# Optimization experiments

Hardware: AMD Instinct MI355X
Metric: run time of the kernel (lower is better)

## Reference

```python
import jax, jax.numpy as jnp
import numpy as np

D_MODEL = 512
NUM_HEADS = 8
BATCH = 2
SEQ = 2048


def setup_inputs() -> dict:
    key = jax.random.key(0)
    ks = jax.random.split(key, 10)
    H = D_MODEL * NUM_HEADS  # concat width = 4096
    scale_in = 1.0 / np.sqrt(D_MODEL)
    scale_h = 1.0 / np.sqrt(H)
    inp = {
        "input_data": jax.random.normal(ks[0], (BATCH, SEQ, D_MODEL), dtype=jnp.float32),
        # causal mask, broadcastable to [n, h, q, k]; masked_fill where mask == 0
        "mask": jnp.tril(jnp.ones((SEQ, SEQ), dtype=jnp.int32))[None, None, :, :],
        "Wq": jax.random.normal(ks[1], (D_MODEL, H), dtype=jnp.float32) * scale_in,
        "bq": jnp.zeros((H,), dtype=jnp.float32),
        "Wk": jax.random.normal(ks[2], (D_MODEL, H), dtype=jnp.float32) * scale_in,
        "bk": jnp.zeros((H,), dtype=jnp.float32),
        "Wv": jax.random.normal(ks[3], (D_MODEL, H), dtype=jnp.float32) * scale_in,
        "bv": jnp.zeros((H,), dtype=jnp.float32),
        "Wo": jax.random.normal(ks[4], (H, D_MODEL), dtype=jnp.float32) * scale_h,
        "bo": jnp.zeros((D_MODEL,), dtype=jnp.float32),
    }
    return inp


def reference(input_data, mask, Wq, bq, Wk, bk, Wv, bv, Wo, bo):
    n, s, d_model = input_data.shape
    H = Wq.shape[1] // d_model  # num_heads; per-head dim == d_model in this module
    q = (input_data @ Wq + bq).reshape(n, s, H, d_model)
    k = (input_data @ Wk + bk).reshape(n, s, H, d_model)
    v = (input_data @ Wv + bv).reshape(n, s, H, d_model)
    scores = jnp.einsum('nqhd,nkhd->nhqk', q, k) / jnp.sqrt(jnp.float32(d_model))
    scores = jnp.where(mask == 0, jnp.float32(-1e9), scores)
    weights = jax.nn.softmax(scores, axis=-1)
    # Faithful to source: contracts weights over BOTH k and q axes (source quirk)
    output = jnp.einsum('nhkq,nvhd->nvhd', weights, v)
    concat = output.reshape(n, s, H * d_model)
    return concat @ Wo + bo
```

## Files before the change

### kernel.cpp

```cpp
#include <hip/hip_runtime.h>


#define DM 512
#define HC 4096
#define SEQF 2048.0f
#define LDR 40

typedef short bf16x8 __attribute__((ext_vector_type(8)));
typedef float f32x4 __attribute__((ext_vector_type(4)));

__device__ __forceinline__ void split2(float x, ushort& h, ushort& l) {
    unsigned b = __float_as_uint(x);
    h = (ushort)(b >> 16);
    float hf = __uint_as_float((unsigned)h << 16);
    l = (ushort)(__float_as_uint(x - hf) >> 16);
}

__device__ __forceinline__ void stage64_f32(const float* __restrict__ src, int ld,
                                            int row0, int k0, ushort* Hh, ushort* Hl,
                                            int tid) {
    const int r = tid >> 2, co = (tid & 3) * 8;
    const float* p = src + (size_t)(row0 + r) * ld + k0 + co;
    const float4 v0 = *reinterpret_cast<const float4*>(p);
    const float4 v1 = *reinterpret_cast<const float4*>(p + 4);
    ushort4 h0, l0, h1, l1;
    split2(v0.x, h0.x, l0.x); split2(v0.y, h0.y, l0.y);
    split2(v0.z, h0.z, l0.z); split2(v0.w, h0.w, l0.w);
    split2(v1.x, h1.x, l1.x); split2(v1.y, h1.y, l1.y);
    split2(v1.z, h1.z, l1.z); split2(v1.w, h1.w, l1.w);
    *reinterpret_cast<ushort4*>(&Hh[r * LDR + co])     = h0;
    *reinterpret_cast<ushort4*>(&Hh[r * LDR + co + 4]) = h1;
    *reinterpret_cast<ushort4*>(&Hl[r * LDR + co])     = l0;
    *reinterpret_cast<ushort4*>(&Hl[r * LDR + co + 4]) = l1;
}

__device__ __forceinline__ void stage64_bf16(const ushort* __restrict__ sh,
                                             const ushort* __restrict__ sl, int ld,
                                             int row0, int k0, ushort* Hh, ushort* Hl,
                                             int tid) {
    const int r = tid >> 2, co = (tid & 3) * 8;
    const size_t off = (size_t)(row0 + r) * ld + k0 + co;
    *reinterpret_cast<int4*>(&Hh[r * LDR + co]) = *reinterpret_cast<const int4*>(&sh[off]);
    *reinterpret_cast<int4*>(&Hl[r * LDR + co]) = *reinterpret_cast<const int4*>(&sl[off]);
}

__global__ __launch_bounds__(256) void prep_wo(const float* __restrict__ Wo,
                                               const float* __restrict__ bv,
                                               ushort* __restrict__ WoTh,
                                               ushort* __restrict__ WoTl,
                                               float* __restrict__ cvec) {
    __shared__ float T[64][65];
    const int bj = blockIdx.x;
    const int bn = blockIdx.y;
    const int tid = threadIdx.x;
    {
        const int r = tid >> 2, c16 = (tid & 3) * 16;
        const float* p = Wo + (size_t)(bj * 64 + r) * DM + bn * 64 + c16;
#pragma unroll
        for (int c = 0; c < 4; ++c) {
            float4 v = *reinterpret_cast<const float4*>(p + c * 4);
            T[r][c16 + c * 4 + 0] = v.x;
            T[r][c16 + c * 4 + 1] = v.y;
            T[r][c16 + c * 4 + 2] = v.z;
            T[r][c16 + c * 4 + 3] = v.w;
        }
    }
    __syncthreads();
    {
        const int rn = tid >> 2, c16 = (tid & 3) * 16;
        const size_t off = (size_t)(bn * 64 + rn) * HC + bj * 64 + c16;
#pragma unroll
        for (int q = 0; q < 4; ++q) {
            ushort4 uh, ul;
            split2(T[c16 + q * 4 + 0][rn], uh.x, ul.x);
            split2(T[c16 + q * 4 + 1][rn], uh.y, ul.y);
            split2(T[c16 + q * 4 + 2][rn], uh.z, ul.z);
            split2(T[c16 + q * 4 + 3][rn], uh.w, ul.w);
            *reinterpret_cast<ushort4*>(&WoTh[off + q * 4]) = uh;
            *reinterpret_cast<ushort4*>(&WoTl[off + q * 4]) = ul;
        }
    }
    if (tid < 64) {
        float s = 0.f;
#pragma unroll 8
        for (int j = 0; j < 64; ++j) s = fmaf(bv[bj * 64 + j], T[j][tid], s);
        atomicAdd(&cvec[bn * 64 + tid], SEQF * s);
    }
}

__global__ __launch_bounds__(256) void gemm_wcT(const ushort* __restrict__ WoTh,
                                                const ushort* __restrict__ WoTl,
                                                const float* __restrict__ Wv,
                                                float* __restrict__ WcT) {
    __shared__ ushort Ah[64 * LDR], Al[64 * LDR], Bh[64 * LDR], Bl[64 * LDR];
    const int d = blockIdx.x;
    const int lin = (d & 7) * 64 + (d >> 3);
    const int kc = lin >> 6, tile = lin & 63;
    const int nt = tile >> 3, it = tile & 7;
    const int a0 = nt * 64, b0 = it * 64, kb = kc * 512;
    const int tid = threadIdx.x, wave = tid >> 6, lane = tid & 63;
    const int wm = wave * 16, fr = lane & 15, fs = (lane >> 4) * 8;

    f32x4 acc[4] = {};
    for (int t = 0; t < 16; ++t) {
        const int k0 = kb + t * 32;
        stage64_bf16(WoTh, WoTl, HC, a0, k0, Ah, Al, tid);
        stage64_f32(Wv, HC, b0, k0, Bh, Bl, tid);
        __syncthreads();
        const int ai = (wm + fr) * LDR + fs;
        const bf16x8 ah = *reinterpret_cast<const bf16x8*>(&Ah[ai]);
        const bf16x8 al = *reinterpret_cast<const bf16x8*>(&Al[ai]);
#pragma unroll
        for (int g = 0; g < 4; ++g) {
            const int bi = (g * 16 + fr) * LDR + fs;
            const bf16x8 bh = *reinterpret_cast<const bf16x8*>(&Bh[bi]);
            const bf16x8 bl = *reinterpret_cast<const bf16x8*>(&Bl[bi]);
            acc[g] = __builtin_amdgcn_mfma_f32_16x16x32_bf16(ah, bh, acc[g], 0, 0, 0);
            acc[g] = __builtin_amdgcn_mfma_f32_16x16x32_bf16(ah, bl, acc[g], 0, 0, 0);
            acc[g] = __builtin_amdgcn_mfma_f32_16x16x32_bf16(al, bh, acc[g], 0, 0, 0);
        }
        __syncthreads();
    }
#pragma unroll
    for (int g = 0; g < 4; ++g)
#pragma unroll
        for (int q = 0; q < 4; ++q) {
            const int row = a0 + wm + (lane >> 4) * 4 + q;
            const int col = b0 + g * 16 + (lane & 15);
            atomicAdd(&WcT[(size_t)row * DM + col], SEQF * acc[g][q]);
        }
}

__global__ __launch_bounds__(256) void gemm_out(const float* __restrict__ X,
                                                const float* __restrict__ WcT,
                                                const float* __restrict__ cvec,
                                                const float* __restrict__ bo,
                                                float* __restrict__ out) {
    __shared__ ushort Ah[64 * LDR], Al[64 * LDR], Bh[64 * LDR], Bl[64 * LDR];
    const int d = blockIdx.x;
    const int lin = (d & 7) * 64 + (d >> 3);
    const int mt = lin >> 3, nt = lin & 7;
    const int a0 = mt * 64, b0 = nt * 64;
    const int tid = threadIdx.x, wave = tid >> 6, lane = tid & 63;
    const int wm = wave * 16, fr = lane & 15, fs = (lane >> 4) * 8;

    f32x4 acc[4] = {};
    for (int t = 0; t < 16; ++t) {
        const int k0 = t * 32;
        stage64_f32(X, DM, a0, k0, Ah, Al, tid);
        stage64_f32(WcT, DM, b0, k0, Bh, Bl, tid);
        __syncthreads();
        const int ai = (wm + fr) * LDR + fs;
        const bf16x8 ah = *reinterpret_cast<const bf16x8*>(&Ah[ai]);
        const bf16x8 al = *reinterpret_cast<const bf16x8*>(&Al[ai]);
#pragma unroll
        for (int g = 0; g < 4; ++g) {
            const int bi = (g * 16 + fr) * LDR + fs;
            const bf16x8 bh = *reinterpret_cast<const bf16x8*>(&Bh[bi]);
            const bf16x8 bl = *reinterpret_cast<const bf16x8*>(&Bl[bi]);
            acc[g] = __builtin_amdgcn_mfma_f32_16x16x32_bf16(ah, bh, acc[g], 0, 0, 0);
            acc[g] = __builtin_amdgcn_mfma_f32_16x16x32_bf16(ah, bl, acc[g], 0, 0, 0);
            acc[g] = __builtin_amdgcn_mfma_f32_16x16x32_bf16(al, bh, acc[g], 0, 0, 0);
        }
        __syncthreads();
    }
#pragma unroll
    for (int g = 0; g < 4; ++g) {
        const int n = b0 + g * 16 + (lane & 15);
        const float cb = cvec[n] + bo[n];
#pragma unroll
        for (int q = 0; q < 4; ++q) {
            const int m = a0 + wm + (lane >> 4) * 4 + q;
            out[(size_t)m * DM + n] = acc[g][q] + cb;
        }
    }
}

extern "C" void kernel_launch(void* const* d_in, const int* in_sizes, int n_in,
                              void* d_out, int out_size, void* d_ws, size_t ws_size,
                              hipStream_t stream) {
    const float* input = (const float*)d_in[0];
    const float* Wv    = (const float*)d_in[6];
    const float* bv    = (const float*)d_in[7];
    const float* Wo    = (const float*)d_in[8];
    const float* bo    = (const float*)d_in[9];
    float* out = (float*)d_out;

    ushort* WoTh = (ushort*)d_ws;
    ushort* WoTl = WoTh + (size_t)DM * HC;
    float*  WcT  = (float*)(WoTl + (size_t)DM * HC);
    float*  cvec = WcT + (size_t)DM * DM;

    hipMemsetAsync(WcT, 0, (size_t)DM * DM * 4 + DM * 4, stream);

    prep_wo<<<dim3(64, 8), 256, 0, stream>>>(Wo, bv, WoTh, WoTl, cvec);
    gemm_wcT<<<512, 256, 0, stream>>>(WoTh, WoTl, Wv, WcT);
    gemm_out<<<512, 256, 0, stream>>>(input, WcT, cvec, bo, out);
}
```

Before: 154.4 us.

## Fuse memset, Wo prep and both GEMMs into one cooperative kernel with grid syncs

Replaces the memset and three separate kernel launches with a single cooperative kernel that zeroes the workspace, transposes and splits Wo, computes WcT, then computes the output, with grid-wide syncs between phases. The GEMM loops now prefetch the next K tile into registers while the current tile is computed, a register-level software pipeline. The bias-vector reduction moves into the second phase and reads the bf16 hi/lo split of Wo from global memory. This removes launch overhead and inter-kernel gaps, at the cost of grid-sync overhead and a hard requirement that all 512 blocks are co-resident.

```diff
diff --git a/kernel.cpp b/kernel.cpp
--- a/kernel.cpp
+++ b/kernel.cpp
@@ -1,4 +1,7 @@
 #include <hip/hip_runtime.h>
+#include <hip/hip_cooperative_groups.h>
+
+namespace cg = cooperative_groups;
 
 
 #define DM 512
@@ -15,163 +18,201 @@
     float hf = __uint_as_float((unsigned)h << 16);
     l = (ushort)(__float_as_uint(x - hf) >> 16);
 }
-
-__device__ __forceinline__ void stage64_f32(const float* __restrict__ src, int ld,
-                                            int row0, int k0, ushort* Hh, ushort* Hl,
-                                            int tid) {
+__device__ __forceinline__ float bf2f(ushort u) {
+    return __uint_as_float((unsigned)u << 16);
+}
+
+__global__ __launch_bounds__(256) void fused_mha(
+    const float* __restrict__ X, const float* __restrict__ Wv,
+    const float* __restrict__ bv, const float* __restrict__ Wo,
+    const float* __restrict__ bo, ushort* __restrict__ WoTh,
+    ushort* __restrict__ WoTl, float* __restrict__ WcT,
+    float* __restrict__ cvec, float* __restrict__ out) {
+    __shared__ alignas(16) unsigned char smem[20480];
+    ushort* Ah = (ushort*)smem;
+    ushort* Al = Ah + 2560;
+    ushort* Bh = Al + 2560;
+    ushort* Bl = Bh + 2560;
+
+    const int bid = blockIdx.x, tid = threadIdx.x;
+    const int lane = tid & 63, wave = tid >> 6;
+    const int wm = wave * 16, fr = lane & 15, fs = (lane >> 4) * 8;
     const int r = tid >> 2, co = (tid & 3) * 8;
-    const float* p = src + (size_t)(row0 + r) * ld + k0 + co;
-    const float4 v0 = *reinterpret_cast<const float4*>(p);
-    const float4 v1 = *reinterpret_cast<const float4*>(p + 4);
-    ushort4 h0, l0, h1, l1;
-    split2(v0.x, h0.x, l0.x); split2(v0.y, h0.y, l0.y);
-    split2(v0.z, h0.z, l0.z); split2(v0.w, h0.w, l0.w);
-    split2(v1.x, h1.x, l1.x); split2(v1.y, h1.y, l1.y);
-    split2(v1.z, h1.z, l1.z); split2(v1.w, h1.w, l1.w);
-    *reinterpret_cast<ushort4*>(&Hh[r * LDR + co])     = h0;
-    *reinterpret_cast<ushort4*>(&Hh[r * LDR + co + 4]) = h1;
-    *reinterpret_cast<ushort4*>(&Hl[r * LDR + co])     = l0;
-    *reinterpret_cast<ushort4*>(&Hl[r * LDR + co + 4]) = l1;
-}
-
-__device__ __forceinline__ void stage64_bf16(const ushort* __restrict__ sh,
-                                             const ushort* __restrict__ sl, int ld,
-                                             int row0, int k0, ushort* Hh, ushort* Hl,
-                                             int tid) {
-    const int r = tid >> 2, co = (tid & 3) * 8;
-    const size_t off = (size_t)(row0 + r) * ld + k0 + co;
-    *reinterpret_cast<int4*>(&Hh[r * LDR + co]) = *reinterpret_cast<const int4*>(&sh[off]);
-    *reinterpret_cast<int4*>(&Hl[r * LDR + co]) = *reinterpret_cast<const int4*>(&sl[off]);
-}
-
-__global__ __launch_bounds__(256) void prep_wo(const float* __restrict__ Wo,
-                                               const float* __restrict__ bv,
-                                               ushort* __restrict__ WoTh,
-                                               ushort* __restrict__ WoTl,
-                                               float* __restrict__ cvec) {
-    __shared__ float T[64][65];
-    const int bj = blockIdx.x;
-    const int bn = blockIdx.y;
-    const int tid = threadIdx.x;
-    {
-        const int r = tid >> 2, c16 = (tid & 3) * 16;
-        const float* p = Wo + (size_t)(bj * 64 + r) * DM + bn * 64 + c16;
+
+    {
+        const int base = bid * 513;
+        WcT[base + tid] = 0.f;
+        WcT[base + 256 + tid] = 0.f;
+        if (tid == 0) WcT[base + 512] = 0.f;
+    }
+    {
+        float (*T)[65] = (float(*)[65])smem;
+        const int bj = bid & 63, bn = bid >> 6;
+        const int rr = tid >> 2, c16 = (tid & 3) * 16;
+        const float* p = Wo + (size_t)(bj * 64 + rr) * DM + bn * 64 + c16;
 #pragma unroll
         for (int c = 0; c < 4; ++c) {
             float4 v = *reinterpret_cast<const float4*>(p + c * 4);
-            T[r][c16 + c * 4 + 0] = v.x;
-            T[r][c16 + c * 4 + 1] = v.y;
-            T[r][c16 + c * 4 + 2] = v.z;
-            T[r][c16 + c * 4 + 3] = v.w;
-        }
-    }
-    __syncthreads();
-    {
-        const int rn = tid >> 2, c16 = (tid & 3) * 16;
-        const size_t off = (size_t)(bn * 64 + rn) * HC + bj * 64 + c16;
+            T[rr][c16 + c * 4 + 0] = v.x;
+            T[rr][c16 + c * 4 + 1] = v.y;
+            T[rr][c16 + c * 4 + 2] = v.z;
+            T[rr][c16 + c * 4 + 3] = v.w;
+        }
+        __syncthreads();
+        const size_t off = (size_t)(bn * 64 + rr) * HC + bj * 64 + c16;
 #pragma unroll
         for (int q = 0; q < 4; ++q) {
             ushort4 uh, ul;
-            split2(T[c16 + q * 4 + 0][rn], uh.x, ul.x);
-            split2(T[c16 + q * 4 + 1][rn], uh.y, ul.y);
-            split2(T[c16 + q * 4 + 2][rn], uh.z, ul.z);
-            split2(T[c16 + q * 4 + 3][rn], uh.w, ul.w);
+            split2(T[c16 + q * 4 + 0][rr], uh.x, ul.x);
+            split2(T[c16 + q * 4 + 1][rr], uh.y, ul.y);
+            split2(T[c16 + q * 4 + 2][rr], uh.z, ul.z);
+            split2(T[c16 + q * 4 + 3][rr], uh.w, ul.w);
             *reinterpret_cast<ushort4*>(&WoTh[off + q * 4]) = uh;
             *reinterpret_cast<ushort4*>(&WoTl[off + q * 4]) = ul;
         }
     }
-    if (tid < 64) {
-        float s = 0.f;
+    cg::this_grid().sync();
+
+    {
+        const int lin = (bid & 7) * 64 + (bid >> 3);
+        const int kc = lin >> 6, tile = lin & 63;
+        const int nt = tile >> 3, it = tile & 7;
+        const int a0 = nt * 64, b0 = it * 64, kb = kc * 512;
+        const size_t aoff = (size_t)(a0 + r) * HC + co;
+        const float* bp = Wv + (size_t)(b0 + r) * HC + co;
+
+        int4 rah = *reinterpret_cast<const int4*>(&WoTh[aoff + kb]);
+        int4 ral = *reinterpret_cast<const int4*>(&WoTl[aoff + kb]);
+        float4 rb0 = *reinterpret_cast<const float4*>(bp + kb);
+        float4 rb1 = *reinterpret_cast<const float4*>(bp + kb + 4);
+        auto stash = [&]() {
+            *reinterpret_cast<int4*>(&Ah[r * LDR + co]) = rah;
+            *reinterpret_cast<int4*>(&Al[r * LDR + co]) = ral;
+            ushort4 h0, l0, h1, l1;
+            split2(rb0.x, h0.x, l0.x); split2(rb0.y, h0.y, l0.y);
+            split2(rb0.z, h0.z, l0.z); split2(rb0.w, h0.w, l0.w);
+            split2(rb1.x, h1.x, l1.x); split2(rb1.y, h1.y, l1.y);
+            split2(rb1.z, h1.z, l1.z); split2(rb1.w, h1.w, l1.w);
+            *reinterpret_cast<ushort4*>(&Bh[r * LDR + co])     = h0;
+            *reinterpret_cast<ushort4*>(&Bh[r * LDR + co + 4]) = h1;
+            *reinterpret_cast<ushort4*>(&Bl[r * LDR + co])     = l0;
+            *reinterpret_cast<ushort4*>(&Bl[r * LDR + co + 4]) = l1;
+        };
+        stash();
+        __syncthreads();
+        f32x4 acc[4] = {};
+        for (int t = 0; t < 16; ++t) {
+            if (t < 15) {
+                const int k1 = kb + (t + 1) * 32;
+                rah = *reinterpret_cast<const int4*>(&WoTh[aoff + k1]);
+                ral = *reinterpret_cast<const int4*>(&WoTl[aoff + k1]);
+                rb0 = *reinterpret_cast<const float4*>(bp + k1);
+                rb1 = *reinterpret_cast<const float4*>(bp + k1 + 4);
+            }
+            const int ai = (wm + fr) * LDR + fs;
+            const bf16x8 ah = *reinterpret_cast<const bf16x8*>(&Ah[ai]);
+            const bf16x8 al = *reinterpret_cast<const bf16x8*>(&Al[ai]);
+#pragma unroll
+            for (int g = 0; g < 4; ++g) {
+                const int bi = (g * 16 + fr) * LDR + fs;
+                const bf16x8 bh = *reinterpret_cast<const bf16x8*>(&Bh[bi]);
+                const bf16x8 bl = *reinterpret_cast<const bf16x8*>(&Bl[bi]);
+                acc[g] = __builtin_amdgcn_mfma_f32_16x16x32_bf16(ah, bh, acc[g], 0, 0, 0);
+                acc[g] = __builtin_amdgcn_mfma_f32_16x16x32_bf16(ah, bl, acc[g], 0, 0, 0);
+                acc[g] = __builtin_amdgcn_mfma_f32_16x16x32_bf16(al, bh, acc[g], 0, 0, 0);
+            }
+            __syncthreads();
+            if (t < 15) stash();
+            __syncthreads();
+        }
+#pragma unroll
+        for (int g = 0; g < 4; ++g)
+#pragma unroll
+            for (int q = 0; q < 4; ++q) {
+                const int row = a0 + wm + (lane >> 4) * 4 + q;
+                const int col = b0 + g * 16 + (lane & 15);
+                atomicAdd(&WcT[(size_t)row * DM + col], SEQF * acc[g][q]);
+            }
+        if (tid < 64) {
+            const int jb = kb + it * 64;
+            float s = 0.f;
 #pragma unroll 8
-        for (int j = 0; j < 64; ++j) s = fmaf(bv[bj * 64 + j], T[j][tid], s);
-        atomicAdd(&cvec[bn * 64 + tid], SEQF * s);
-    }
-}
-
-__global__ __launch_bounds__(256) void gemm_wcT(const ushort* __restrict__ WoTh,
-                                                const ushort* __restrict__ WoTl,
-                                                const float* __restrict__ Wv,
-                                                float* __restrict__ WcT) {
-    __shared__ ushort Ah[64 * LDR], Al[64 * LDR], Bh[64 * LDR], Bl[64 * LDR];
-    const int d = blockIdx.x;
-    const int lin = (d & 7) * 64 + (d >> 3);
-    const int kc = lin >> 6, tile = lin & 63;
-    const int nt = tile >> 3, it = tile & 7;
-    const int a0 = nt * 64, b0 = it * 64, kb = kc * 512;
-    const int tid = threadIdx.x, wave = tid >> 6, lane = tid & 63;
-    const int wm = wave * 16, fr = lane & 15, fs = (lane >> 4) * 8;
-
-    f32x4 acc[4] = {};
-    for (int t = 0; t < 16; ++t) {
-        const int k0 = kb + t * 32;
-        stage64_bf16(WoTh, WoTl, HC, a0, k0, Ah, Al, tid);
-        stage64_f32(Wv, HC, b0, k0, Bh, Bl, tid);
+            for (int jj = 0; jj < 64; ++jj) {
+                const int j = jb + jj;
+                const size_t o = (size_t)(a0 + tid) * HC + j;
+                s = fmaf(bv[j], bf2f(WoTh[o]) + bf2f(WoTl[o]), s);
+            }
+            atomicAdd(&cvec[a0 + tid], SEQF * s);
+        }
+    }
+    cg::this_grid().sync();
+
+    {
+        const int lin = (bid & 7) * 64 + (bid >> 3);
+        const int mt = lin >> 3, nt = lin & 7;
+        const int a0 = mt * 64, b0 = nt * 64;
+        const float* ap = X + (size_t)(a0 + r) * DM + co;
+        const float* bp = WcT + (size_t)(b0 + r) * DM + co;
+
+        float4 ra0 = *reinterpret_cast<const float4*>(ap);
+        float4 ra1 = *reinterpret_cast<const float4*>(ap + 4);
+        float4 rb0 = *reinterpret_cast<const float4*>(bp);
+        float4 rb1 = *reinterpret_cast<const float4*>(bp + 4);
+        auto stash = [&]() {
+            ushort4 h, l;
+            split2(ra0.x, h.x, l.x); split2(ra0.y, h.y, l.y);
+            split2(ra0.z, h.z, l.z); split2(ra0.w, h.w, l.w);
+            *reinterpret_cast<ushort4*>(&Ah[r * LDR + co]) = h;
+            *reinterpret_cast<ushort4*>(&Al[r * LDR + co]) = l;
+            split2(ra1.x, h.x, l.x); split2(ra1.y, h.y, l.y);
+            split2(ra1.z, h.z, l.z); split2(ra1.w, h.w, l.w);
+            *reinterpret_cast<ushort4*>(&Ah[r * LDR + co + 4]) = h;
+            *reinterpret_cast<ushort4*>(&Al[r * LDR + co + 4]) = l;
+            split2(rb0.x, h.x, l.x); split2(rb0.y, h.y, l.y);
+            split2(rb0.z, h.z, l.z); split2(rb0.w, h.w, l.w);
+            *reinterpret_cast<ushort4*>(&Bh[r * LDR + co]) = h;
+            *reinterpret_cast<ushort4*>(&Bl[r * LDR + co]) = l;
+            split2(rb1.x, h.x, l.x); split2(rb1.y, h.y, l.y);
+            split2(rb1.z, h.z, l.z); split2(rb1.w, h.w, l.w);
+            *reinterpret_cast<ushort4*>(&Bh[r * LDR + co + 4]) = h;
+            *reinterpret_cast<ushort4*>(&Bl[r * LDR + co + 4]) = l;
+        };
+        stash();
         __syncthreads();
-        const int ai = (wm + fr) * LDR + fs;
-        const bf16x8 ah = *reinterpret_cast<const bf16x8*>(&Ah[ai]);
-        const bf16x8 al = *reinterpret_cast<const bf16x8*>(&Al[ai]);
+        f32x4 acc[4] = {};
+        for (int t = 0; t < 16; ++t) {
+            if (t < 15) {
+                const int k1 = (t + 1) * 32;
+                ra0 = *reinterpret_cast<const float4*>(ap + k1);
+                ra1 = *reinterpret_cast<const float4*>(ap + k1 + 4);
+                rb0 = *reinterpret_cast<const float4*>(bp + k1);
+                rb1 = *reinterpret_cast<const float4*>(bp + k1 + 4);
+            }
+            const int ai = (wm + fr) * LDR + fs;
+            const bf16x8 ah = *reinterpret_cast<const bf16x8*>(&Ah[ai]);
+            const bf16x8 al = *reinterpret_cast<const bf16x8*>(&Al[ai]);
+#pragma unroll
+            for (int g = 0; g < 4; ++g) {
+                const int bi = (g * 16 + fr) * LDR + fs;
+                const bf16x8 bh = *reinterpret_cast<const bf16x8*>(&Bh[bi]);
+                const bf16x8 bl = *reinterpret_cast<const bf16x8*>(&Bl[bi]);
+                acc[g] = __builtin_amdgcn_mfma_f32_16x16x32_bf16(ah, bh, acc[g], 0, 0, 0);
+                acc[g] = __builtin_amdgcn_mfma_f32_16x16x32_bf16(ah, bl, acc[g], 0, 0, 0);
+                acc[g] = __builtin_amdgcn_mfma_f32_16x16x32_bf16(al, bh, acc[g], 0, 0, 0);
+            }
+            __syncthreads();
+            if (t < 15) stash();
+            __syncthreads();
+        }
 #pragma unroll
         for (int g = 0; g < 4; ++g) {
-            const int bi = (g * 16 + fr) * LDR + fs;
-            const bf16x8 bh = *reinterpret_cast<const bf16x8*>(&Bh[bi]);
-            const bf16x8 bl = *reinterpret_cast<const bf16x8*>(&Bl[bi]);
-            acc[g] = __builtin_amdgcn_mfma_f32_16x16x32_bf16(ah, bh, acc[g], 0, 0, 0);
-            acc[g] = __builtin_amdgcn_mfma_f32_16x16x32_bf16(ah, bl, acc[g], 0, 0, 0);
-            acc[g] = __builtin_amdgcn_mfma_f32_16x16x32_bf16(al, bh, acc[g], 0, 0, 0);
-        }
-        __syncthreads();
-    }
-#pragma unroll
-    for (int g = 0; g < 4; ++g)
-#pragma unroll
-        for (int q = 0; q < 4; ++q) {
-            const int row = a0 + wm + (lane >> 4) * 4 + q;
-            const int col = b0 + g * 16 + (lane & 15);
-            atomicAdd(&WcT[(size_t)row * DM + col], SEQF * acc[g][q]);
-        }
-}
-
-__global__ __launch_bounds__(256) void gemm_out(const float* __restrict__ X,
-                                                const float* __restrict__ WcT,
-                                                const float* __restrict__ cvec,
-                                                const float* __restrict__ bo,
-                                                float* __restrict__ out) {
-    __shared__ ushort Ah[64 * LDR], Al[64 * LDR], Bh[64 * LDR], Bl[64 * LDR];
-    const int d = blockIdx.x;
-    const int lin = (d & 7) * 64 + (d >> 3);
-    const int mt = lin >> 3, nt = lin & 7;
-    const int a0 = mt * 64, b0 = nt * 64;
-    const int tid = threadIdx.x, wave = tid >> 6, lane = tid & 63;
-    const int wm = wave * 16, fr = lane & 15, fs = (lane >> 4) * 8;
-
-    f32x4 acc[4] = {};
-    for (int t = 0; t < 16; ++t) {
-        const int k0 = t * 32;
-        stage64_f32(X, DM, a0, k0, Ah, Al, tid);
-        stage64_f32(WcT, DM, b0, k0, Bh, Bl, tid);
-        __syncthreads();
-        const int ai = (wm + fr) * LDR + fs;
-        const bf16x8 ah = *reinterpret_cast<const bf16x8*>(&Ah[ai]);
-        const bf16x8 al = *reinterpret_cast<const bf16x8*>(&Al[ai]);
-#pragma unroll
-        for (int g = 0; g < 4; ++g) {
-            const int bi = (g * 16 + fr) * LDR + fs;
-            const bf16x8 bh = *reinterpret_cast<const bf16x8*>(&Bh[bi]);
-            const bf16x8 bl = *reinterpret_cast<const bf16x8*>(&Bl[bi]);
-            acc[g] = __builtin_amdgcn_mfma_f32_16x16x32_bf16(ah, bh, acc[g], 0, 0, 0);
-            acc[g] = __builtin_amdgcn_mfma_f32_16x16x32_bf16(ah, bl, acc[g], 0, 0, 0);
-            acc[g] = __builtin_amdgcn_mfma_f32_16x16x32_bf16(al, bh, acc[g], 0, 0, 0);
-        }
-        __syncthreads();
-    }
-#pragma unroll
-    for (int g = 0; g < 4; ++g) {
-        const int n = b0 + g * 16 + (lane & 15);
-        const float cb = cvec[n] + bo[n];
-#pragma unroll
-        for (int q = 0; q < 4; ++q) {
-            const int m = a0 + wm + (lane >> 4) * 4 + q;
-            out[(size_t)m * DM + n] = acc[g][q] + cb;
+            const int n = b0 + g * 16 + (lane & 15);
+            const float cb = cvec[n] + bo[n];
+#pragma unroll
+            for (int q = 0; q < 4; ++q) {
+                const int m = a0 + wm + (lane >> 4) * 4 + q;
+                out[(size_t)m * DM + n] = acc[g][q] + cb;
+            }
         }
     }
 }
@@ -179,11 +220,11 @@
 extern "C" void kernel_launch(void* const* d_in, const int* in_sizes, int n_in,
                               void* d_out, int out_size, void* d_ws, size_t ws_size,
                               hipStream_t stream) {
-    const float* input = (const float*)d_in[0];
-    const float* Wv    = (const float*)d_in[6];
-    const float* bv    = (const float*)d_in[7];
-    const float* Wo    = (const float*)d_in[8];
-    const float* bo    = (const float*)d_in[9];
+    const float* X  = (const float*)d_in[0];
+    const float* Wv = (const float*)d_in[6];
+    const float* bv = (const float*)d_in[7];
+    const float* Wo = (const float*)d_in[8];
+    const float* bo = (const float*)d_in[9];
     float* out = (float*)d_out;
 
     ushort* WoTh = (ushort*)d_ws;
@@ -191,9 +232,7 @@
     float*  WcT  = (float*)(WoTl + (size_t)DM * HC);
     float*  cvec = WcT + (size_t)DM * DM;
 
-    hipMemsetAsync(WcT, 0, (size_t)DM * DM * 4 + DM * 4, stream);
-
-    prep_wo<<<dim3(64, 8), 256, 0, stream>>>(Wo, bv, WoTh, WoTl, cvec);
-    gemm_wcT<<<512, 256, 0, stream>>>(WoTh, WoTl, Wv, WcT);
-    gemm_out<<<512, 256, 0, stream>>>(input, WcT, cvec, bo, out);
-}
+    void* args[] = {(void*)&X, (void*)&Wv, (void*)&bv, (void*)&Wo, (void*)&bo,
+                    (void*)&WoTh, (void*)&WoTl, (void*)&WcT, (void*)&cvec, (void*)&out};
+    hipLaunchCooperativeKernel(fused_mha, dim3(512), dim3(256), args, 0, stream);
+}
```

Result: slower. 273.6 us (+77.1%).

## Fuse Wo transpose/split and bias vector into the Wc GEMM kernel

Applied to the files above, without the earlier changes.

Removes the separate prep_wo kernel that transposed Wo into bf16 hi/lo workspace arrays. gemm_wcT now reads fp32 Wo directly, splits it into hi/lo and writes it transposed into shared memory while staging. The cvec bias term is computed by the it==7 blocks. This saves a launch and a round trip of the bf16 copies through global memory. In exchange it adds transposed shared-memory stores that may hit bank conflicts, and makes the blocks with it==7 do extra serial work.

```diff
diff --git a/kernel.cpp b/kernel.cpp
--- a/kernel.cpp
+++ b/kernel.cpp
@@ -34,64 +34,11 @@
     *reinterpret_cast<ushort4*>(&Hl[r * LDR + co + 4]) = l1;
 }
 
-__device__ __forceinline__ void stage64_bf16(const ushort* __restrict__ sh,
-                                             const ushort* __restrict__ sl, int ld,
-                                             int row0, int k0, ushort* Hh, ushort* Hl,
-                                             int tid) {
-    const int r = tid >> 2, co = (tid & 3) * 8;
-    const size_t off = (size_t)(row0 + r) * ld + k0 + co;
-    *reinterpret_cast<int4*>(&Hh[r * LDR + co]) = *reinterpret_cast<const int4*>(&sh[off]);
-    *reinterpret_cast<int4*>(&Hl[r * LDR + co]) = *reinterpret_cast<const int4*>(&sl[off]);
-}
-
-__global__ __launch_bounds__(256) void prep_wo(const float* __restrict__ Wo,
-                                               const float* __restrict__ bv,
-                                               ushort* __restrict__ WoTh,
-                                               ushort* __restrict__ WoTl,
-                                               float* __restrict__ cvec) {
-    __shared__ float T[64][65];
-    const int bj = blockIdx.x;
-    const int bn = blockIdx.y;
-    const int tid = threadIdx.x;
-    {
-        const int r = tid >> 2, c16 = (tid & 3) * 16;
-        const float* p = Wo + (size_t)(bj * 64 + r) * DM + bn * 64 + c16;
-#pragma unroll
-        for (int c = 0; c < 4; ++c) {
-            float4 v = *reinterpret_cast<const float4*>(p + c * 4);
-            T[r][c16 + c * 4 + 0] = v.x;
-            T[r][c16 + c * 4 + 1] = v.y;
-            T[r][c16 + c * 4 + 2] = v.z;
-            T[r][c16 + c * 4 + 3] = v.w;
-        }
-    }
-    __syncthreads();
-    {
-        const int rn = tid >> 2, c16 = (tid & 3) * 16;
-        const size_t off = (size_t)(bn * 64 + rn) * HC + bj * 64 + c16;
-#pragma unroll
-        for (int q = 0; q < 4; ++q) {
-            ushort4 uh, ul;
-            split2(T[c16 + q * 4 + 0][rn], uh.x, ul.x);
-            split2(T[c16 + q * 4 + 1][rn], uh.y, ul.y);
-            split2(T[c16 + q * 4 + 2][rn], uh.z, ul.z);
-            split2(T[c16 + q * 4 + 3][rn], uh.w, ul.w);
-            *reinterpret_cast<ushort4*>(&WoTh[off + q * 4]) = uh;
-            *reinterpret_cast<ushort4*>(&WoTl[off + q * 4]) = ul;
-        }
-    }
-    if (tid < 64) {
-        float s = 0.f;
-#pragma unroll 8
-        for (int j = 0; j < 64; ++j) s = fmaf(bv[bj * 64 + j], T[j][tid], s);
-        atomicAdd(&cvec[bn * 64 + tid], SEQF * s);
-    }
-}
-
-__global__ __launch_bounds__(256) void gemm_wcT(const ushort* __restrict__ WoTh,
-                                                const ushort* __restrict__ WoTl,
+__global__ __launch_bounds__(256) void gemm_wcT(const float* __restrict__ Wo,
                                                 const float* __restrict__ Wv,
-                                                float* __restrict__ WcT) {
+                                                const float* __restrict__ bv,
+                                                float* __restrict__ WcT,
+                                                float* __restrict__ cvec) {
     __shared__ ushort Ah[64 * LDR], Al[64 * LDR], Bh[64 * LDR], Bl[64 * LDR];
     const int d = blockIdx.x;
     const int lin = (d & 7) * 64 + (d >> 3);
@@ -100,11 +47,24 @@
     const int a0 = nt * 64, b0 = it * 64, kb = kc * 512;
     const int tid = threadIdx.x, wave = tid >> 6, lane = tid & 63;
     const int wm = wave * 16, fr = lane & 15, fs = (lane >> 4) * 8;
+    const int jr = tid >> 3, nc = (tid & 7) * 8;
 
     f32x4 acc[4] = {};
     for (int t = 0; t < 16; ++t) {
         const int k0 = kb + t * 32;
-        stage64_bf16(WoTh, WoTl, HC, a0, k0, Ah, Al, tid);
+        {
+            const float* p = Wo + (size_t)(k0 + jr) * DM + a0 + nc;
+            const float4 v0 = *reinterpret_cast<const float4*>(p);
+            const float4 v1 = *reinterpret_cast<const float4*>(p + 4);
+            const float w[8] = {v0.x, v0.y, v0.z, v0.w, v1.x, v1.y, v1.z, v1.w};
+#pragma unroll
+            for (int q = 0; q < 8; ++q) {
+                ushort h, l;
+                split2(w[q], h, l);
+                Ah[(nc + q) * LDR + jr] = h;
+                Al[(nc + q) * LDR + jr] = l;
+            }
+        }
         stage64_f32(Wv, HC, b0, k0, Bh, Bl, tid);
         __syncthreads();
         const int ai = (wm + fr) * LDR + fs;
@@ -129,6 +89,15 @@
             const int col = b0 + g * 16 + (lane & 15);
             atomicAdd(&WcT[(size_t)row * DM + col], SEQF * acc[g][q]);
         }
+    if (it == 7) {
+        const int n = a0 + (tid & 63);
+        const int jseg = kb + (tid >> 6) * 128;
+        float s = 0.f;
+#pragma unroll 8
+        for (int jj = 0; jj < 128; ++jj)
+            s = fmaf(bv[jseg + jj], Wo[(size_t)(jseg + jj) * DM + n], s);
+        atomicAdd(&cvec[n], SEQF * s);
+    }
 }
 
 __global__ __launch_bounds__(256) void gemm_out(const float* __restrict__ X,
@@ -179,21 +148,18 @@
 extern "C" void kernel_launch(void* const* d_in, const int* in_sizes, int n_in,
                               void* d_out, int out_size, void* d_ws, size_t ws_size,
                               hipStream_t stream) {
-    const float* input = (const float*)d_in[0];
-    const float* Wv    = (const float*)d_in[6];
-    const float* bv    = (const float*)d_in[7];
-    const float* Wo    = (const float*)d_in[8];
-    const float* bo    = (const float*)d_in[9];
+    const float* X  = (const float*)d_in[0];
+    const float* Wv = (const float*)d_in[6];
+    const float* bv = (const float*)d_in[7];
+    const float* Wo = (const float*)d_in[8];
+    const float* bo = (const float*)d_in[9];
     float* out = (float*)d_out;
 
-    ushort* WoTh = (ushort*)d_ws;
-    ushort* WoTl = WoTh + (size_t)DM * HC;
-    float*  WcT  = (float*)(WoTl + (size_t)DM * HC);
-    float*  cvec = WcT + (size_t)DM * DM;
+    float* WcT  = (float*)d_ws;
+    float* cvec = WcT + (size_t)DM * DM;
 
     hipMemsetAsync(WcT, 0, (size_t)DM * DM * 4 + DM * 4, stream);
 
-    prep_wo<<<dim3(64, 8), 256, 0, stream>>>(Wo, bv, WoTh, WoTl, cvec);
-    gemm_wcT<<<512, 256, 0, stream>>>(WoTh, WoTl, Wv, WcT);
-    gemm_out<<<512, 256, 0, stream>>>(input, WcT, cvec, bo, out);
+    gemm_wcT<<<512, 256, 0, stream>>>(Wo, Wv, bv, WcT, cvec);
+    gemm_out<<<512, 256, 0, stream>>>(X, WcT, cvec, bo, out);
 }
```

Result: slower. 158.1 us (+2.4%).
